# Optimization experiments

Hardware: AMD Instinct MI355X
Metric: run time of the kernel (lower is better)

Reference implementation:

```python
import jax, jax.numpy as jnp
import numpy as np

B, S, H = 4, 2048, 1024
D_FF = 4 * H
NUM_EXPERTS = 8
TOP_K = 2


def setup_inputs() -> dict:
    key = jax.random.key(0)
    ks = jax.random.split(key, 6)
    scale = 0.02
    return {
        "hidden_states": jax.random.normal(ks[0], (B, S, H), dtype=jnp.float32),
        "w_router": jax.random.normal(ks[1], (NUM_EXPERTS, H), dtype=jnp.float32) * scale,
        "w1": jax.random.normal(ks[2], (NUM_EXPERTS, D_FF, H), dtype=jnp.float32) * scale,
        "b1": jnp.zeros((NUM_EXPERTS, D_FF), dtype=jnp.float32),
        "w2": jax.random.normal(ks[3], (NUM_EXPERTS, H, D_FF), dtype=jnp.float32) * scale,
        "b2": jnp.zeros((NUM_EXPERTS, H), dtype=jnp.float32),
    }


def reference(hidden_states, w_router, w1, b1, w2, b2):
    Bc, Sc, Hc = hidden_states.shape
    E = w_router.shape[0]
    dtype = hidden_states.dtype

    # Router: logits [B, S, E], top-k, softmax over the k selected logits.
    router_logits = jnp.einsum("bsh,eh->bse", hidden_states, w_router)
    topk_values, topk_indices = jax.lax.top_k(router_logits, TOP_K)
    topk_weights = jax.nn.softmax(topk_values.astype(jnp.float32), axis=-1).astype(dtype)

    # Per-token combine weight for each expert: [B, S, E] -> [T, E].
    # (Equivalent to the torch sort/group + weighted index_add_ combine.)
    combine = jnp.sum(
        jax.nn.one_hot(topk_indices, E, dtype=dtype) * topk_weights[..., None], axis=-2
    )
    flat = hidden_states.reshape(-1, Hc)          # [T, H]
    cw = combine.reshape(-1, E)                    # [T, E]

    # Dense-equivalent MoE: each expert MLP runs on all tokens, scaled by its
    # combine weight (zero for unrouted tokens) -> identical math to gather/scatter.
    mixed = jnp.zeros_like(flat)
    for e in range(E):
        h1 = jax.nn.gelu(flat @ w1[e].T + b1[e], approximate=False)  # [T, 4H]
        mixed = mixed + cw[:, e:e + 1] * (h1 @ w2[e].T + b2[e])
    return mixed.reshape(Bc, Sc, Hc)
```

## Files before the change

kernel.cpp:

```cpp
#include <hip/hip_runtime.h>
#include <hip/hip_bf16.h>
#include <math.h>


#define TT  8192
#define HD  1024
#define DFF 4096
#define NE  8
#define ROWCAP 18432
#define MAXT 72

typedef __attribute__((ext_vector_type(8))) short short8;
typedef __attribute__((ext_vector_type(4))) float f32x4;

static __device__ __forceinline__ unsigned short f2bf(float f) {
    unsigned int u = __float_as_uint(f);
    unsigned int r = (u + 0x7fffu + ((u >> 16) & 1u)) >> 16;
    return (unsigned short)r;
}

static __device__ __forceinline__ float bf2f(unsigned short u) {
    return __uint_as_float((unsigned int)u << 16);
}

static __device__ __forceinline__ float gelu_fast(float v) {
    const float s = v * (1.5957691f + 0.07135481f * v * v);
    return v / (1.f + __expf(-s));
}

static __device__ __forceinline__ void gload_lds16(const void* gp, void* lp) {
    __builtin_amdgcn_global_load_lds(
        (__attribute__((address_space(1))) void*)(void*)gp,
        (__attribute__((address_space(3))) void*)lp,
        16, 0, 0);
}

#define BARM                                        \
    __builtin_amdgcn_s_barrier();                   \
    asm volatile("" ::: "memory");                  \
    __builtin_amdgcn_sched_barrier(0)
#define LGKM0                                       \
    asm volatile("s_waitcnt lgkmcnt(0)" ::: "memory"); \
    __builtin_amdgcn_sched_barrier(0)
#define PRIO1 __builtin_amdgcn_s_setprio(1)
#define PRIO0 __builtin_amdgcn_s_setprio(0)

__global__ __launch_bounds__(256) void cvt_w2_kernel(const float* __restrict__ s1,
                                                     unsigned short* __restrict__ d1,
                                                     const float* __restrict__ s2,
                                                     unsigned short* __restrict__ d2,
                                                     long n4) {
    for (long i = (long)blockIdx.x * 256 + threadIdx.x; i < 2 * n4;
         i += (long)gridDim.x * 256) {
        const bool second = i >= n4;
        const long j = second ? i - n4 : i;
        float4 v = second ? ((const float4*)s2)[j] : ((const float4*)s1)[j];
        ushort4 o;
        o.x = f2bf(v.x); o.y = f2bf(v.y); o.z = f2bf(v.z); o.w = f2bf(v.w);
        if (second) ((ushort4*)d2)[j] = o; else ((ushort4*)d1)[j] = o;
    }
}

__global__ __launch_bounds__(256) void cvt_w_kernel(const float* __restrict__ s,
                                                    unsigned short* __restrict__ d,
                                                    long n4) {
    for (long i = (long)blockIdx.x * 256 + threadIdx.x; i < n4;
         i += (long)gridDim.x * 256) {
        float4 v = ((const float4*)s)[i];
        ushort4 o;
        o.x = f2bf(v.x); o.y = f2bf(v.y); o.z = f2bf(v.z); o.w = f2bf(v.w);
        ((ushort4*)d)[i] = o;
    }
}

__global__ __launch_bounds__(256) void router_kernel(const float* __restrict__ x,
                                                     const float* __restrict__ wr,
                                                     int* __restrict__ tokE,
                                                     float* __restrict__ tokW,
                                                     int* __restrict__ counts) {
    __shared__ float wrs[NE * HD];
    const int tid = threadIdx.x;
#pragma unroll
    for (int i = 0; i < NE * HD / 4 / 256; ++i)
        ((float4*)wrs)[i * 256 + tid] = ((const float4*)wr)[i * 256 + tid];
    __syncthreads();

    const int token = blockIdx.x * 4 + (tid >> 6);
    const int lane = tid & 63;
    const float* xp = x + (long)token * HD;
    double lg[NE];
#pragma unroll
    for (int e = 0; e < NE; ++e) lg[e] = 0.0;
    for (int i = lane; i < HD; i += 64) {
        const double xv = (double)xp[i];
#pragma unroll
        for (int e = 0; e < NE; ++e) lg[e] += xv * (double)wrs[e * HD + i];
    }
#pragma unroll
    for (int e = 0; e < NE; ++e) {
        double s = lg[e];
#pragma unroll
        for (int off = 32; off > 0; off >>= 1) s += __shfl_xor(s, off, 64);
        lg[e] = s;
    }
    if (lane == 0) {
        int i0 = 0; double v0 = lg[0];
#pragma unroll
        for (int e = 1; e < NE; ++e) if (lg[e] > v0) { v0 = lg[e]; i0 = e; }
        int i1 = -1; double v1 = -1e300;
#pragma unroll
        for (int e = 0; e < NE; ++e) if (e != i0 && lg[e] > v1) { v1 = lg[e]; i1 = e; }
        double p = exp(v1 - v0);
        double d = 1.0 + p;
        tokE[token * 2] = i0;     tokW[token * 2] = (float)(1.0 / d);
        tokE[token * 2 + 1] = i1; tokW[token * 2 + 1] = (float)(p / d);
        atomicAdd(&counts[i0], 1);
        atomicAdd(&counts[i1], 1);
    }
}

__global__ __launch_bounds__(256) void init_setup_kernel(const int* __restrict__ counts,
                                                         int* __restrict__ cursor,
                                                         int* __restrict__ tE,
                                                         int* __restrict__ tR,
                                                         int* __restrict__ rowTok) {
    const int i = blockIdx.x * 256 + threadIdx.x;
    if (i < ROWCAP) rowTok[i] = 0;
    if (blockIdx.x == gridDim.x - 1 && threadIdx.x == 0) {
        int off = 0, t = 0;
        for (int e = 0; e < NE; ++e) {
            cursor[e] = off;
            const int padded = (counts[e] + 255) & ~255;
            for (int j = 0; j < padded / 256; ++j) {
                tE[t] = e; tR[t] = off + j * 256; ++t;
            }
            off += padded;
        }
        for (; t < MAXT; ++t) tE[t] = -1;
    }
}

__global__ __launch_bounds__(256) void scatter_kernel(const int* __restrict__ tokE,
                                                      int* __restrict__ cursor,
                                                      int* __restrict__ rowTok,
                                                      int* __restrict__ posOf) {
    const int t = blockIdx.x * 256 + threadIdx.x;
#pragma unroll
    for (int j = 0; j < 2; ++j) {
        const int e = tokE[t * 2 + j];
        const int pos = atomicAdd(&cursor[e], 1);
        rowTok[pos] = t;
        posOf[t * 2 + j] = pos;
    }
}

__global__ __launch_bounds__(256) void gather_kernel(const float* __restrict__ x,
                                                     const int* __restrict__ rowTok,
                                                     unsigned short* __restrict__ Xg) {
    const int row = blockIdx.x;
    const int tok = rowTok[row];
    const float4 v = ((const float4*)(x + (long)tok * HD))[threadIdx.x];
    ushort4 o;
    o.x = f2bf(v.x); o.y = f2bf(v.y); o.z = f2bf(v.z); o.w = f2bf(v.w);
    ((ushort4*)(Xg + (long)row * HD))[threadIdx.x] = o;
}

template <int EPI, int N, int K, int BN>
__global__ __launch_bounds__(512, 2) void gemm4p(
    const unsigned short* __restrict__ A,
    const unsigned short* __restrict__ W,
    const int* __restrict__ tE,
    const int* __restrict__ tR,
    unsigned short* __restrict__ Hout,
    const float* __restrict__ bias) {
    constexpr int BM = 256, BK = 64, NT = K / BK;
    constexpr int NREP = BN / 64;
    constexpr int NREP2 = NREP / 2;
    constexpr int NB = BN / 64;
    constexpr int NB2 = NB / 2;
    constexpr int HB = BN / 8;
    constexpr int LOG2HB = (BN == 256) ? 5 : 4;
    constexpr int VB = NB2 + 2;
    constexpr int AHALF = BM * BK;
    constexpr int HALF = (BM + BN) * BK;

    const int nwg = gridDim.x * gridDim.y;
    int bid = blockIdx.y * gridDim.x + blockIdx.x;
    bid = (bid & 7) * (nwg >> 3) + (bid >> 3);
    const int tix = bid % gridDim.x;
    const int niy = bid / gridDim.x;

    const int e = tE[tix];
    if (e < 0) return;

    __shared__ unsigned short smem[2 * HALF];

    const int tid = threadIdx.x;
    const int lane = tid & 63;
    const int quad = lane >> 4;
    const int l15 = lane & 15;
    const int wid = tid >> 6;
    const int wrr = wid >> 2;
    const int wcc = wid & 3;

    const long row0 = tR[tix];
    const long n0 = (long)niy * BN;
    const unsigned short* Ab = A + row0 * K;
    const unsigned short* Bb = W + ((long)e * N + n0) * K;

    const unsigned short* aS[4];
    int aD[4];
#pragma unroll
    for (int i = 0; i < 4; ++i) {
        const int c = i * 512 + tid;
        const int r = c >> 3, s = c & 7;
        aS[i] = Ab + (long)r * K + (s ^ (r & 7)) * 8;
        aD[i] = c * 8;
    }
    const unsigned short* bS[NB];
    int bD[NB];
#pragma unroll
    for (int i = 0; i < NB; ++i) {
        const int c = i * 512 + tid;
        const int rho = c >> 3, s = c & 7;
        const int rl = rho & (BN / 2 - 1);
        const int r = (rl & (HB - 1)) + ((rl >> LOG2HB) << (LOG2HB + 1)) +
                      ((rho >= BN / 2) ? HB : 0);
        bS[i] = Bb + (long)r * K + (s ^ (rho & 7)) * 8;
        bD[i] = c * 8;
    }

    auto stgA = [&](int buf, int t, int g) {
        unsigned short* dst = smem + buf * HALF;
        gload_lds16(aS[g] + (long)t * BK, dst + aD[g]);
        gload_lds16(aS[g + 2] + (long)t * BK, dst + aD[g + 2]);
    };
    auto stgB = [&](int buf, int t, int g) {
        unsigned short* dst = smem + buf * HALF + AHALF;
#pragma unroll
        for (int j = 0; j < NB2; ++j)
            gload_lds16(bS[g * NB2 + j] + (long)t * BK, dst + bD[g * NB2 + j]);
    };
    auto rdA = [&](const unsigned short* Ac, int mi, int ks) -> short8 {
        const int row = wrr * 128 + mi * 16 + l15;
        return *(const short8*)(Ac + row * BK + ((ks * 4 + quad) ^ (row & 7)) * 8);
    };
    auto rdB = [&](const unsigned short* Bc, int ni, int ks) -> short8 {
        int rho;
        if constexpr (BN == 256)
            rho = (ni & 1) * 16 + l15 + wcc * 32 + ((ni & 2) ? 128 : 0);
        else
            rho = l15 + wcc * 16 + ni * 64;
        return *(const short8*)(Bc + rho * BK + ((ks * 4 + quad) ^ (rho & 7)) * 8);
    };

#define RD_A(AF, AC, HM)                                                \
    _Pragma("unroll") for (int i_ = 0; i_ < 4; ++i_)                    \
    _Pragma("unroll") for (int k_ = 0; k_ < 2; ++k_)                    \
        AF[i_][k_] = rdA(AC, (HM) * 4 + i_, k_);
#define RD_B(BF, BC, HN)                                                \
    _Pragma("unroll") for (int j_ = 0; j_ < NREP2; ++j_)                \
    _Pragma("unroll") for (int k_ = 0; k_ < 2; ++k_)                    \
        BF[j_][k_] = rdB(BC, (HN) * NREP2 + j_, k_);
#define MMA_Q(AF, BF, HM, HN)                                           \
    _Pragma("unroll") for (int i_ = 0; i_ < 4; ++i_)                    \
    _Pragma("unroll") for (int j_ = 0; j_ < NREP2; ++j_)                \
    _Pragma("unroll") for (int k_ = 0; k_ < 2; ++k_)                    \
        acc[(HM) * 4 + i_][(HN) * NREP2 + j_] =                         \
            __builtin_amdgcn_mfma_f32_16x16x32_bf16(                    \
                AF[i_][k_], BF[j_][k_],                                 \
                acc[(HM) * 4 + i_][(HN) * NREP2 + j_], 0, 0, 0);
#define VMC(NN) asm volatile("s_waitcnt vmcnt(%0)" ::"n"(NN) : "memory")

    f32x4 acc[8][NREP];
#pragma unroll
    for (int i = 0; i < 8; ++i)
#pragma unroll
        for (int j = 0; j < NREP; ++j) acc[i][j] = (f32x4){0.f, 0.f, 0.f, 0.f};

    stgA(0, 0, 0); stgB(0, 0, 0); stgA(0, 0, 1); stgB(0, 0, 1);
    VMC(VB);
    BARM;

#pragma unroll 1
    for (int t = 0; t < NT - 1; ++t) {
        const int cur = t & 1;
        const int nb = cur ^ 1;
        const unsigned short* Ac = smem + cur * HALF;
        const unsigned short* Bc = Ac + AHALF;
        short8 af0[4][2], af1[4][2], bf0[NREP2][2], bf1[NREP2][2];
        RD_A(af0, Ac, 0); RD_B(bf0, Bc, 0);
        stgA(nb, t + 1, 0);
        BARM; LGKM0;
        PRIO1; MMA_Q(af0, bf0, 0, 0); PRIO0;
        VMC(VB); BARM;
        RD_A(af1, Ac, 1);
        stgB(nb, t + 1, 0);
        BARM; LGKM0;
        PRIO1; MMA_Q(af1, bf0, 1, 0); PRIO0;
        VMC(VB); BARM;
        RD_B(bf1, Bc, 1);
        stgA(nb, t + 1, 1);
        BARM; LGKM0;
        PRIO1; MMA_Q(af1, bf1, 1, 1); PRIO0;
        BARM;
        stgB(nb, t + 1, 1);
        BARM;
        PRIO1; MMA_Q(af0, bf1, 0, 1); PRIO0;
        VMC(VB); BARM;
    }

    {
        const int cur = (NT - 1) & 1;
        const unsigned short* Ac = smem + cur * HALF;
        const unsigned short* Bc = Ac + AHALF;
        short8 af0[4][2], af1[4][2], bf0[NREP2][2], bf1[NREP2][2];
        RD_A(af0, Ac, 0); RD_B(bf0, Bc, 0);
        BARM; LGKM0;
        PRIO1; MMA_Q(af0, bf0, 0, 0); PRIO0;
        VMC(NB2); BARM;
        RD_A(af1, Ac, 1);
        BARM; LGKM0;
        PRIO1; MMA_Q(af1, bf0, 1, 0); PRIO0;
        VMC(0); BARM;
        RD_B(bf1, Bc, 1);
        BARM; LGKM0;
        PRIO1; MMA_Q(af1, bf1, 1, 1); PRIO0;
        PRIO1; MMA_Q(af0, bf1, 0, 1); PRIO0;
    }

#pragma unroll
    for (int mi = 0; mi < 8; ++mi) {
        const long grow0 = row0 + wrr * 128 + mi * 16 + quad * 4;
#pragma unroll
        for (int ni = 0; ni < NREP; ++ni) {
            const long col = n0 + wcc * (BN / 4) + ni * 16 + l15;
            const float bcol = bias[(long)e * N + col];
#pragma unroll
            for (int r = 0; r < 4; ++r) {
                float v = acc[mi][ni][r] + bcol;
                if constexpr (EPI == 0) v = gelu_fast(v);
                Hout[(grow0 + r) * N + col] = f2bf(v);
            }
        }
    }
#undef RD_A
#undef RD_B
#undef MMA_Q
#undef VMC
}

__global__ __launch_bounds__(256) void combine_kernel(const unsigned short* __restrict__ Y,
                                                      const int* __restrict__ posOf,
                                                      const float* __restrict__ tokW,
                                                      float* __restrict__ out) {
    const int t = blockIdx.x;
    const int p0 = posOf[t * 2];
    const int p1 = posOf[t * 2 + 1];
    const float w0 = tokW[t * 2];
    const float w1 = tokW[t * 2 + 1];
    const ushort4 a = ((const ushort4*)(Y + (long)p0 * HD))[threadIdx.x];
    const ushort4 b = ((const ushort4*)(Y + (long)p1 * HD))[threadIdx.x];
    float4 o;
    o.x = w0 * bf2f(a.x) + w1 * bf2f(b.x);
    o.y = w0 * bf2f(a.y) + w1 * bf2f(b.y);
    o.z = w0 * bf2f(a.z) + w1 * bf2f(b.z);
    o.w = w0 * bf2f(a.w) + w1 * bf2f(b.w);
    ((float4*)(out + (long)t * HD))[threadIdx.x] = o;
}

extern "C" void kernel_launch(void* const* d_in, const int* in_sizes, int n_in,
                              void* d_out, int out_size, void* d_ws, size_t ws_size,
                              hipStream_t stream) {
    const float* x  = (const float*)d_in[0];
    const float* wr = (const float*)d_in[1];
    const float* w1 = (const float*)d_in[2];
    const float* b1 = (const float*)d_in[3];
    const float* w2 = (const float*)d_in[4];
    const float* b2 = (const float*)d_in[5];
    float* out = (float*)d_out;

    const size_t WBYTES = (size_t)NE * DFF * HD * 2;
    const bool full = ws_size >= (size_t)326 * 1024 * 1024;

    char* p = (char*)d_ws;
    auto alloc = [&](size_t bytes) {
        char* r = p;
        p += (bytes + 255) & ~(size_t)255;
        return r;
    };
    unsigned short* Xg  = (unsigned short*)alloc((size_t)ROWCAP * HD * 2);
    unsigned short* H1g = (unsigned short*)alloc((size_t)ROWCAP * DFF * 2);
    unsigned short* Wb1 = (unsigned short*)alloc(WBYTES);
    unsigned short* Wb2 = full ? (unsigned short*)alloc(WBYTES) : Wb1;
    int*   rowTok  = (int*)alloc((size_t)ROWCAP * 4);
    int*   posOf   = (int*)alloc((size_t)TT * 2 * 4);
    int*   tokE    = (int*)alloc((size_t)TT * 2 * 4);
    float* tokW    = (float*)alloc((size_t)TT * 2 * 4);
    int*   counts  = (int*)alloc(64);
    int*   cursor  = (int*)alloc(64);
    int*   tE      = (int*)alloc(MAXT * 4);
    int*   tR      = (int*)alloc(MAXT * 4);

    unsigned short* Yg = Xg;

    hipMemsetAsync(counts, 0, 64, stream);

    const long n4w = (long)NE * DFF * HD / 4;
    if (full) {
        cvt_w2_kernel<<<dim3(8192), dim3(256), 0, stream>>>(w1, Wb1, w2, Wb2, n4w);
    } else {
        cvt_w_kernel<<<dim3(4096), dim3(256), 0, stream>>>(w1, Wb1, n4w);
    }

    router_kernel<<<dim3(TT / 4), dim3(256), 0, stream>>>(x, wr, tokE, tokW, counts);
    init_setup_kernel<<<dim3(ROWCAP / 256 + 1), dim3(256), 0, stream>>>(
        counts, cursor, tE, tR, rowTok);
    scatter_kernel<<<dim3(TT / 256), dim3(256), 0, stream>>>(tokE, cursor, rowTok, posOf);
    gather_kernel<<<dim3(ROWCAP), dim3(256), 0, stream>>>(x, rowTok, Xg);

    gemm4p<0, DFF, HD, 256><<<dim3(MAXT, DFF / 256), dim3(512), 0, stream>>>(
        Xg, Wb1, tE, tR, H1g, b1);

    if (!full)
        cvt_w_kernel<<<dim3(4096), dim3(256), 0, stream>>>(w2, Wb1, n4w);
    gemm4p<1, HD, DFF, 128><<<dim3(MAXT, HD / 128), dim3(512), 0, stream>>>(
        H1g, Wb2, tE, tR, Yg, b2);

    combine_kernel<<<dim3(TT), dim3(256), 0, stream>>>(Yg, posOf, tokW, out);
}
```

Before: 1.015 ms.

## Fuse preprocessing into one cooperative kernel and add dedicated second-GEMM kernel

Replaces the weight-conversion, router, setup, scatter and gather launches with a single cooperative kernel that uses grid-wide syncs between phases. This removes several kernel launches and the memset. The second expert GEMM moves to a new dedicated kernel with a 2-stage pipeline and a simpler BN=128 tile schedule. The cooperative grid of 512 blocks does the weight conversion with fewer threads, which may run slower than the wide launch it replaces, and the grid syncs add their own cost.

```diff
diff --git a/kernel.cpp b/kernel.cpp
--- a/kernel.cpp
+++ b/kernel.cpp
@@ -1,6 +1,9 @@
 #include <hip/hip_runtime.h>
+#include <hip/hip_cooperative_groups.h>
 #include <hip/hip_bf16.h>
 #include <math.h>
+
+namespace cg = cooperative_groups;
 
 
 #define TT  8192
@@ -44,20 +47,114 @@
     __builtin_amdgcn_sched_barrier(0)
 #define PRIO1 __builtin_amdgcn_s_setprio(1)
 #define PRIO0 __builtin_amdgcn_s_setprio(0)
-
-__global__ __launch_bounds__(256) void cvt_w2_kernel(const float* __restrict__ s1,
-                                                     unsigned short* __restrict__ d1,
-                                                     const float* __restrict__ s2,
-                                                     unsigned short* __restrict__ d2,
-                                                     long n4) {
-    for (long i = (long)blockIdx.x * 256 + threadIdx.x; i < 2 * n4;
-         i += (long)gridDim.x * 256) {
-        const bool second = i >= n4;
-        const long j = second ? i - n4 : i;
-        float4 v = second ? ((const float4*)s2)[j] : ((const float4*)s1)[j];
+#define VMC(NN) asm volatile("s_waitcnt vmcnt(%0)" ::"n"(NN) : "memory")
+
+__global__ __launch_bounds__(256, 2) void prep_kernel(
+    const float* __restrict__ x, const float* __restrict__ wr,
+    const float* __restrict__ w1, const float* __restrict__ w2,
+    unsigned short* __restrict__ Wb1, unsigned short* __restrict__ Wb2,
+    int* __restrict__ tokE, float* __restrict__ tokW,
+    int* __restrict__ counts, int* __restrict__ cursor,
+    int* __restrict__ tE, int* __restrict__ tR,
+    int* __restrict__ rowTok, int* __restrict__ posOf,
+    unsigned short* __restrict__ Xg, int doW2) {
+    cg::grid_group grid = cg::this_grid();
+    const int tid = threadIdx.x;
+    const long gt = (long)blockIdx.x * 256 + tid;
+    const long gsz = (long)gridDim.x * 256;
+
+    if (gt < NE) counts[gt] = 0;
+    const long n4 = (long)NE * DFF * HD / 4;
+    for (long i = gt; i < n4; i += gsz) {
+        float4 v = ((const float4*)w1)[i];
         ushort4 o;
         o.x = f2bf(v.x); o.y = f2bf(v.y); o.z = f2bf(v.z); o.w = f2bf(v.w);
-        if (second) ((ushort4*)d2)[j] = o; else ((ushort4*)d1)[j] = o;
+        ((ushort4*)Wb1)[i] = o;
+        if (doW2) {
+            float4 u = ((const float4*)w2)[i];
+            ushort4 q;
+            q.x = f2bf(u.x); q.y = f2bf(u.y); q.z = f2bf(u.z); q.w = f2bf(u.w);
+            ((ushort4*)Wb2)[i] = q;
+        }
+    }
+    __threadfence();
+    grid.sync();
+
+    __shared__ float wrs[NE * HD];
+#pragma unroll
+    for (int i = 0; i < NE * HD / 4 / 256; ++i)
+        ((float4*)wrs)[i * 256 + tid] = ((const float4*)wr)[i * 256 + tid];
+    __syncthreads();
+    const int lane = tid & 63;
+    for (int token = blockIdx.x * 4 + (tid >> 6); token < TT; token += gridDim.x * 4) {
+        const float* xp = x + (long)token * HD;
+        double lg[NE];
+#pragma unroll
+        for (int e = 0; e < NE; ++e) lg[e] = 0.0;
+        for (int i = lane; i < HD; i += 64) {
+            const double xv = (double)xp[i];
+#pragma unroll
+            for (int e = 0; e < NE; ++e) lg[e] += xv * (double)wrs[e * HD + i];
+        }
+#pragma unroll
+        for (int e = 0; e < NE; ++e) {
+            double s = lg[e];
+#pragma unroll
+            for (int off = 32; off > 0; off >>= 1) s += __shfl_xor(s, off, 64);
+            lg[e] = s;
+        }
+        if (lane == 0) {
+            int i0 = 0; double v0 = lg[0];
+#pragma unroll
+            for (int e = 1; e < NE; ++e) if (lg[e] > v0) { v0 = lg[e]; i0 = e; }
+            int i1 = -1; double v1 = -1e300;
+#pragma unroll
+            for (int e = 0; e < NE; ++e) if (e != i0 && lg[e] > v1) { v1 = lg[e]; i1 = e; }
+            double p = exp(v1 - v0);
+            double d = 1.0 + p;
+            tokE[token * 2] = i0;     tokW[token * 2] = (float)(1.0 / d);
+            tokE[token * 2 + 1] = i1; tokW[token * 2 + 1] = (float)(p / d);
+            atomicAdd(&counts[i0], 1);
+            atomicAdd(&counts[i1], 1);
+        }
+    }
+    __threadfence();
+    grid.sync();
+
+    for (long i = gt; i < ROWCAP; i += gsz) rowTok[i] = 0;
+    if (gt == 0) {
+        int off = 0, t = 0;
+        for (int e = 0; e < NE; ++e) {
+            cursor[e] = off;
+            const int padded = (counts[e] + 255) & ~255;
+            for (int j = 0; j < padded / 256; ++j) {
+                tE[t] = e; tR[t] = off + j * 256; ++t;
+            }
+            off += padded;
+        }
+        for (; t < MAXT; ++t) tE[t] = -1;
+    }
+    __threadfence();
+    grid.sync();
+
+    for (long t = gt; t < TT; t += gsz) {
+#pragma unroll
+        for (int j = 0; j < 2; ++j) {
+            const int e = tokE[t * 2 + j];
+            const int pos = atomicAdd(&cursor[e], 1);
+            rowTok[pos] = (int)t;
+            posOf[t * 2 + j] = pos;
+        }
+    }
+    __threadfence();
+    grid.sync();
+
+    for (int row = blockIdx.x; row < ROWCAP; row += gridDim.x) {
+        const int tok = rowTok[row];
+        const float4 v = ((const float4*)(x + (long)tok * HD))[tid];
+        ushort4 o;
+        o.x = f2bf(v.x); o.y = f2bf(v.y); o.z = f2bf(v.z); o.w = f2bf(v.w);
+        ((ushort4*)(Xg + (long)row * HD))[tid] = o;
     }
 }
 
@@ -71,98 +168,6 @@
         o.x = f2bf(v.x); o.y = f2bf(v.y); o.z = f2bf(v.z); o.w = f2bf(v.w);
         ((ushort4*)d)[i] = o;
     }
-}
-
-__global__ __launch_bounds__(256) void router_kernel(const float* __restrict__ x,
-                                                     const float* __restrict__ wr,
-                                                     int* __restrict__ tokE,
-                                                     float* __restrict__ tokW,
-                                                     int* __restrict__ counts) {
-    __shared__ float wrs[NE * HD];
-    const int tid = threadIdx.x;
-#pragma unroll
-    for (int i = 0; i < NE * HD / 4 / 256; ++i)
-        ((float4*)wrs)[i * 256 + tid] = ((const float4*)wr)[i * 256 + tid];
-    __syncthreads();
-
-    const int token = blockIdx.x * 4 + (tid >> 6);
-    const int lane = tid & 63;
-    const float* xp = x + (long)token * HD;
-    double lg[NE];
-#pragma unroll
-    for (int e = 0; e < NE; ++e) lg[e] = 0.0;
-    for (int i = lane; i < HD; i += 64) {
-        const double xv = (double)xp[i];
-#pragma unroll
-        for (int e = 0; e < NE; ++e) lg[e] += xv * (double)wrs[e * HD + i];
-    }
-#pragma unroll
-    for (int e = 0; e < NE; ++e) {
-        double s = lg[e];
-#pragma unroll
-        for (int off = 32; off > 0; off >>= 1) s += __shfl_xor(s, off, 64);
-        lg[e] = s;
-    }
-    if (lane == 0) {
-        int i0 = 0; double v0 = lg[0];
-#pragma unroll
-        for (int e = 1; e < NE; ++e) if (lg[e] > v0) { v0 = lg[e]; i0 = e; }
-        int i1 = -1; double v1 = -1e300;
-#pragma unroll
-        for (int e = 0; e < NE; ++e) if (e != i0 && lg[e] > v1) { v1 = lg[e]; i1 = e; }
-        double p = exp(v1 - v0);
-        double d = 1.0 + p;
-        tokE[token * 2] = i0;     tokW[token * 2] = (float)(1.0 / d);
-        tokE[token * 2 + 1] = i1; tokW[token * 2 + 1] = (float)(p / d);
-        atomicAdd(&counts[i0], 1);
-        atomicAdd(&counts[i1], 1);
-    }
-}
-
-__global__ __launch_bounds__(256) void init_setup_kernel(const int* __restrict__ counts,
-                                                         int* __restrict__ cursor,
-                                                         int* __restrict__ tE,
-                                                         int* __restrict__ tR,
-                                                         int* __restrict__ rowTok) {
-    const int i = blockIdx.x * 256 + threadIdx.x;
-    if (i < ROWCAP) rowTok[i] = 0;
-    if (blockIdx.x == gridDim.x - 1 && threadIdx.x == 0) {
-        int off = 0, t = 0;
-        for (int e = 0; e < NE; ++e) {
-            cursor[e] = off;
-            const int padded = (counts[e] + 255) & ~255;
-            for (int j = 0; j < padded / 256; ++j) {
-                tE[t] = e; tR[t] = off + j * 256; ++t;
-            }
-            off += padded;
-        }
-        for (; t < MAXT; ++t) tE[t] = -1;
-    }
-}
-
-__global__ __launch_bounds__(256) void scatter_kernel(const int* __restrict__ tokE,
-                                                      int* __restrict__ cursor,
-                                                      int* __restrict__ rowTok,
-                                                      int* __restrict__ posOf) {
-    const int t = blockIdx.x * 256 + threadIdx.x;
-#pragma unroll
-    for (int j = 0; j < 2; ++j) {
-        const int e = tokE[t * 2 + j];
-        const int pos = atomicAdd(&cursor[e], 1);
-        rowTok[pos] = t;
-        posOf[t * 2 + j] = pos;
-    }
-}
-
-__global__ __launch_bounds__(256) void gather_kernel(const float* __restrict__ x,
-                                                     const int* __restrict__ rowTok,
-                                                     unsigned short* __restrict__ Xg) {
-    const int row = blockIdx.x;
-    const int tok = rowTok[row];
-    const float4 v = ((const float4*)(x + (long)tok * HD))[threadIdx.x];
-    ushort4 o;
-    o.x = f2bf(v.x); o.y = f2bf(v.y); o.z = f2bf(v.z); o.w = f2bf(v.w);
-    ((ushort4*)(Xg + (long)row * HD))[threadIdx.x] = o;
 }
 
 template <int EPI, int N, int K, int BN>
@@ -270,7 +275,6 @@
             __builtin_amdgcn_mfma_f32_16x16x32_bf16(                    \
                 AF[i_][k_], BF[j_][k_],                                 \
                 acc[(HM) * 4 + i_][(HN) * NREP2 + j_], 0, 0, 0);
-#define VMC(NN) asm volatile("s_waitcnt vmcnt(%0)" ::"n"(NN) : "memory")
 
     f32x4 acc[8][NREP];
 #pragma unroll
@@ -347,7 +351,194 @@
 #undef RD_A
 #undef RD_B
 #undef MMA_Q
-#undef VMC
+}
+
+template <int N, int K>
+__global__ __launch_bounds__(512, 2) void gemm2p(
+    const unsigned short* __restrict__ A,
+    const unsigned short* __restrict__ W,
+    const int* __restrict__ tE,
+    const int* __restrict__ tR,
+    unsigned short* __restrict__ Hout,
+    const float* __restrict__ bias) {
+    constexpr int BM = 256, BN = 128, BK = 64, NT = K / BK;
+    constexpr int AHALF = BM * BK;
+    constexpr int HALF = (BM + BN) * BK;
+
+    const int nwg = gridDim.x * gridDim.y;
+    int bid = blockIdx.y * gridDim.x + blockIdx.x;
+    bid = (bid & 7) * (nwg >> 3) + (bid >> 3);
+    const int tix = bid % gridDim.x;
+    const int niy = bid / gridDim.x;
+
+    const int e = tE[tix];
+    if (e < 0) return;
+
+    __shared__ unsigned short smem[2 * HALF];
+
+    const int tid = threadIdx.x;
+    const int lane = tid & 63;
+    const int quad = lane >> 4;
+    const int l15 = lane & 15;
+    const int wid = tid >> 6;
+    const int wrr = wid >> 2;
+    const int wcc = wid & 3;
+
+    const long row0 = tR[tix];
+    const long n0 = (long)niy * BN;
+    const unsigned short* Ab = A + row0 * K;
+    const unsigned short* Bb = W + ((long)e * N + n0) * K;
+
+    const unsigned short* aS[4];
+    int aD[4];
+#pragma unroll
+    for (int i = 0; i < 4; ++i) {
+        const int c = i * 512 + tid;
+        const int r = c >> 3, s = c & 7;
+        aS[i] = Ab + (long)r * K + (s ^ (r & 7)) * 8;
+        aD[i] = c * 8;
+    }
+    const unsigned short* bS[2];
+    int bD[2];
+#pragma unroll
+    for (int i = 0; i < 2; ++i) {
+        const int c = i * 512 + tid;
+        const int r = c >> 3, s = c & 7;
+        bS[i] = Bb + (long)r * K + (s ^ (r & 7)) * 8;
+        bD[i] = c * 8;
+    }
+
+    auto stgA = [&](int buf, int t, int g) {
+        unsigned short* dst = smem + buf * HALF;
+        gload_lds16(aS[g] + (long)t * BK, dst + aD[g]);
+        gload_lds16(aS[g + 2] + (long)t * BK, dst + aD[g + 2]);
+    };
+    auto stgB = [&](int buf, int t) {
+        unsigned short* dst = smem + buf * HALF + AHALF;
+        gload_lds16(bS[0] + (long)t * BK, dst + bD[0]);
+        gload_lds16(bS[1] + (long)t * BK, dst + bD[1]);
+    };
+    auto rdA = [&](const unsigned short* Ac, int mi, int ks) -> short8 {
+        const int row = wrr * 128 + mi * 16 + l15;
+        return *(const short8*)(Ac + row * BK + ((ks * 4 + quad) ^ (row & 7)) * 8);
+    };
+    auto rdB = [&](const unsigned short* Bc, int ni, int ks) -> short8 {
+        const int rho = wcc * 32 + ni * 16 + l15;
+        return *(const short8*)(Bc + rho * BK + ((ks * 4 + quad) ^ (rho & 7)) * 8);
+    };
+
+    f32x4 acc[8][2];
+#pragma unroll
+    for (int i = 0; i < 8; ++i)
+#pragma unroll
+        for (int j = 0; j < 2; ++j) acc[i][j] = (f32x4){0.f, 0.f, 0.f, 0.f};
+
+    stgA(0, 0, 0); stgB(0, 0); stgA(0, 0, 1);
+    VMC(2);
+    BARM;
+
+#pragma unroll 1
+    for (int t = 0; t < NT - 1; ++t) {
+        const int cur = t & 1, nb = cur ^ 1;
+        const unsigned short* Ac = smem + cur * HALF;
+        const unsigned short* Bc = Ac + AHALF;
+        short8 af[4][2], bf[2][2];
+#pragma unroll
+        for (int i = 0; i < 4; ++i)
+#pragma unroll
+            for (int k = 0; k < 2; ++k) af[i][k] = rdA(Ac, i, k);
+#pragma unroll
+        for (int j = 0; j < 2; ++j)
+#pragma unroll
+            for (int k = 0; k < 2; ++k) bf[j][k] = rdB(Bc, j, k);
+        stgA(nb, t + 1, 0); stgB(nb, t + 1);
+        BARM; LGKM0;
+        PRIO1;
+#pragma unroll
+        for (int i = 0; i < 4; ++i)
+#pragma unroll
+            for (int j = 0; j < 2; ++j)
+#pragma unroll
+                for (int k = 0; k < 2; ++k)
+                    acc[i][j] = __builtin_amdgcn_mfma_f32_16x16x32_bf16(
+                        af[i][k], bf[j][k], acc[i][j], 0, 0, 0);
+        PRIO0;
+        VMC(4); BARM;
+#pragma unroll
+        for (int i = 0; i < 4; ++i)
+#pragma unroll
+            for (int k = 0; k < 2; ++k) af[i][k] = rdA(Ac, 4 + i, k);
+        stgA(nb, t + 1, 1);
+        BARM; LGKM0;
+        PRIO1;
+#pragma unroll
+        for (int i = 0; i < 4; ++i)
+#pragma unroll
+            for (int j = 0; j < 2; ++j)
+#pragma unroll
+                for (int k = 0; k < 2; ++k)
+                    acc[4 + i][j] = __builtin_amdgcn_mfma_f32_16x16x32_bf16(
+                        af[i][k], bf[j][k], acc[4 + i][j], 0, 0, 0);
+        PRIO0;
+        VMC(2); BARM;
+    }
+
+    {
+        const int cur = (NT - 1) & 1;
+        const unsigned short* Ac = smem + cur * HALF;
+        const unsigned short* Bc = Ac + AHALF;
+        short8 af[4][2], bf[2][2];
+#pragma unroll
+        for (int i = 0; i < 4; ++i)
+#pragma unroll
+            for (int k = 0; k < 2; ++k) af[i][k] = rdA(Ac, i, k);
+#pragma unroll
+        for (int j = 0; j < 2; ++j)
+#pragma unroll
+            for (int k = 0; k < 2; ++k) bf[j][k] = rdB(Bc, j, k);
+        BARM; LGKM0;
+        PRIO1;
+#pragma unroll
+        for (int i = 0; i < 4; ++i)
+#pragma unroll
+            for (int j = 0; j < 2; ++j)
+#pragma unroll
+                for (int k = 0; k < 2; ++k)
+                    acc[i][j] = __builtin_amdgcn_mfma_f32_16x16x32_bf16(
+                        af[i][k], bf[j][k], acc[i][j], 0, 0, 0);
+        PRIO0;
+        VMC(0); BARM;
+#pragma unroll
+        for (int i = 0; i < 4; ++i)
+#pragma unroll
+            for (int k = 0; k < 2; ++k) af[i][k] = rdA(Ac, 4 + i, k);
+        LGKM0;
+        PRIO1;
+#pragma unroll
+        for (int i = 0; i < 4; ++i)
+#pragma unroll
+            for (int j = 0; j < 2; ++j)
+#pragma unroll
+                for (int k = 0; k < 2; ++k)
+                    acc[4 + i][j] = __builtin_amdgcn_mfma_f32_16x16x32_bf16(
+                        af[i][k], bf[j][k], acc[4 + i][j], 0, 0, 0);
+        PRIO0;
+    }
+
+#pragma unroll
+    for (int mi = 0; mi < 8; ++mi) {
+        const long grow0 = row0 + wrr * 128 + mi * 16 + quad * 4;
+#pragma unroll
+        for (int ni = 0; ni < 2; ++ni) {
+            const long col = n0 + wcc * 32 + ni * 16 + l15;
+            const float bcol = bias[(long)e * N + col];
+#pragma unroll
+            for (int r = 0; r < 4; ++r) {
+                const float v = acc[mi][ni][r] + bcol;
+                Hout[(grow0 + r) * N + col] = f2bf(v);
+            }
+        }
+    }
 }
 
 __global__ __launch_bounds__(256) void combine_kernel(const unsigned short* __restrict__ Y,
@@ -399,33 +590,27 @@
     float* tokW    = (float*)alloc((size_t)TT * 2 * 4);
     int*   counts  = (int*)alloc(64);
     int*   cursor  = (int*)alloc(64);
-    int*   tE      = (int*)alloc(MAXT * 4);
-    int*   tR      = (int*)alloc(MAXT * 4);
+    int*   tEp     = (int*)alloc(MAXT * 4);
+    int*   tRp     = (int*)alloc(MAXT * 4);
 
     unsigned short* Yg = Xg;
 
-    hipMemsetAsync(counts, 0, 64, stream);
-
-    const long n4w = (long)NE * DFF * HD / 4;
-    if (full) {
-        cvt_w2_kernel<<<dim3(8192), dim3(256), 0, stream>>>(w1, Wb1, w2, Wb2, n4w);
-    } else {
-        cvt_w_kernel<<<dim3(4096), dim3(256), 0, stream>>>(w1, Wb1, n4w);
-    }
-
-    router_kernel<<<dim3(TT / 4), dim3(256), 0, stream>>>(x, wr, tokE, tokW, counts);
-    init_setup_kernel<<<dim3(ROWCAP / 256 + 1), dim3(256), 0, stream>>>(
-        counts, cursor, tE, tR, rowTok);
-    scatter_kernel<<<dim3(TT / 256), dim3(256), 0, stream>>>(tokE, cursor, rowTok, posOf);
-    gather_kernel<<<dim3(ROWCAP), dim3(256), 0, stream>>>(x, rowTok, Xg);
+    int doW2 = full ? 1 : 0;
+    void* args[] = {(void*)&x, (void*)&wr, (void*)&w1, (void*)&w2,
+                    (void*)&Wb1, (void*)&Wb2, (void*)&tokE, (void*)&tokW,
+                    (void*)&counts, (void*)&cursor, (void*)&tEp, (void*)&tRp,
+                    (void*)&rowTok, (void*)&posOf, (void*)&Xg, (void*)&doW2};
+    hipLaunchCooperativeKernel((void*)prep_kernel, dim3(512), dim3(256),
+                               args, 0, stream);
 
     gemm4p<0, DFF, HD, 256><<<dim3(MAXT, DFF / 256), dim3(512), 0, stream>>>(
-        Xg, Wb1, tE, tR, H1g, b1);
+        Xg, Wb1, tEp, tRp, H1g, b1);
 
     if (!full)
-        cvt_w_kernel<<<dim3(4096), dim3(256), 0, stream>>>(w2, Wb1, n4w);
-    gemm4p<1, HD, DFF, 128><<<dim3(MAXT, HD / 128), dim3(512), 0, stream>>>(
-        H1g, Wb2, tE, tR, Yg, b2);
+        cvt_w_kernel<<<dim3(4096), dim3(256), 0, stream>>>(
+            w2, Wb1, (long)NE * DFF * HD / 4);
+    gemm2p<HD, DFF><<<dim3(MAXT, HD / 128), dim3(512), 0, stream>>>(
+        H1g, Wb2, tEp, tRp, Yg, b2);
 
     combine_kernel<<<dim3(TT), dim3(256), 0, stream>>>(Yg, posOf, tokW, out);
 }
```

New measurement: 1.362 ms. 34.2% more time.
